# Kernel tuning notes

Hardware: AMD Instinct MI355X
Metric: run time of the kernel (lower is better)

## Reference

```python
import jax, jax.numpy as jnp
import numpy as np

B, N = 32, 512


def _stick_breaking(b, x_mask):
    """Row-major stick-breaking recurrence, O(N^2) sequential steps.

    Equivalent to the TF while_loop: for step in range(N*N), m=step//N, n=step%N:
      fut      = max(0, x_mask[:,m,n+1:] - sum_{m'<m} x[:,m',n+1:])  (col partial sums)
      mfm      = sum_j fut_j
      row_sum  = sum_{n'<n} x[:,m,n']
      col_sum  = sum_{m'<m} x[:,m',n]
      lower    = mask[m,n]*max(0, 1 - row_sum - mfm)
      upper    = mask[m,n]*min(1 - row_sum, 1 - col_sum)
      x[m,n]   = lower + b[m,n]*(upper - lower)
    Key insight: during row m the column partial sums are constant, so the
    future-mass terms for every n can be precomputed as an exclusive reverse
    cumsum; only the within-row dependency (row_sum) needs a scan.
    """
    Bb, Nn, _ = b.shape
    dt = b.dtype

    def row_step(col_sums, inputs):
        b_row, mask_row = inputs                      # [B, N] each
        fut = jnp.maximum(0.0, mask_row - col_sums)   # [B, N]
        # mfm[:, n] = sum_{j > n} fut[:, j]  (exclusive reverse cumsum)
        mfm = jnp.flip(jnp.cumsum(jnp.flip(fut, -1), axis=-1), -1) - fut

        def col_step(row_sum, inp):
            b_mn, m_mn, mfm_n, cs_n = inp             # [B] each
            lower = m_mn * jnp.maximum(0.0, 1.0 - row_sum - mfm_n)
            upper = m_mn * jnp.minimum(1.0 - row_sum, 1.0 - cs_n)
            p = lower + b_mn * (upper - lower)
            return row_sum + p, p

        _, row = jax.lax.scan(
            col_step,
            jnp.zeros((Bb,), dt),
            (b_row.T, mask_row.T, mfm.T, col_sums.T),
        )
        row = row.T                                   # [B, N]
        return col_sums + row, row

    _, rows = jax.lax.scan(
        row_step,
        jnp.zeros((Bb, Nn), dt),
        (jnp.swapaxes(b, 0, 1), jnp.swapaxes(x_mask, 0, 1)),
    )
    return jnp.swapaxes(rows, 0, 1)                   # [B, N, N]


def setup_inputs() -> dict:
    key = jax.random.key(0)
    k1, _ = jax.random.split(key)
    x = jax.random.normal(k1, (B, N, N), dtype=jnp.float32)
    x_mask = jnp.ones((B, N, N), dtype=jnp.float32)
    return {"x": x, "x_mask": x_mask}


def reference(x, x_mask):
    # layer.call applies sigmoid to the logits before stick-breaking
    return _stick_breaking(jax.nn.sigmoid(x), x_mask)
```

## Files before the change

### kernel.cpp

```cpp
#include <hip/hip_runtime.h>

#define NBATCH 32
#define NDIM 512
#define NFAST 448
#define NPAIR 224
#define NWAVE 8


__device__ __forceinline__ float prefix_inc(float x) {
  asm("s_nop 1\n\t"
      "v_add_f32_dpp %0, %0, %0 row_shr:1 row_mask:0xf bank_mask:0xf\n\t"
      "s_nop 1\n\t"
      "v_add_f32_dpp %0, %0, %0 row_shr:2 row_mask:0xf bank_mask:0xf\n\t"
      "s_nop 1\n\t"
      "v_add_f32_dpp %0, %0, %0 row_shr:4 row_mask:0xf bank_mask:0xf\n\t"
      "s_nop 1\n\t"
      "v_add_f32_dpp %0, %0, %0 row_shr:8 row_mask:0xf bank_mask:0xf\n\t"
      "s_nop 1\n\t"
      "v_add_f32_dpp %0, %0, %0 row_bcast:15 row_mask:0xa bank_mask:0xf\n\t"
      "s_nop 1\n\t"
      "v_add_f32_dpp %0, %0, %0 row_bcast:31 row_mask:0xc bank_mask:0xf\n\t"
      "s_nop 1"
      : "+v"(x));
  return x;
}

__device__ __forceinline__ void aff_scan(float& A, float& B) {
  asm("s_nop 1\n\t"
      "v_fmac_f32_dpp %1, %1, %0 row_shr:1 row_mask:0xf bank_mask:0xf\n\t"
      "v_mul_f32_dpp  %0, %0, %0 row_shr:1 row_mask:0xf bank_mask:0xf\n\t"
      "s_nop 0\n\t"
      "v_fmac_f32_dpp %1, %1, %0 row_shr:2 row_mask:0xf bank_mask:0xf\n\t"
      "v_mul_f32_dpp  %0, %0, %0 row_shr:2 row_mask:0xf bank_mask:0xf\n\t"
      "s_nop 0\n\t"
      "v_fmac_f32_dpp %1, %1, %0 row_shr:4 row_mask:0xf bank_mask:0xf\n\t"
      "v_mul_f32_dpp  %0, %0, %0 row_shr:4 row_mask:0xf bank_mask:0xf\n\t"
      "s_nop 0\n\t"
      "v_fmac_f32_dpp %1, %1, %0 row_shr:8 row_mask:0xf bank_mask:0xf\n\t"
      "v_mul_f32_dpp  %0, %0, %0 row_shr:8 row_mask:0xf bank_mask:0xf\n\t"
      "s_nop 0\n\t"
      "v_fmac_f32_dpp %1, %1, %0 row_bcast:15 row_mask:0xa bank_mask:0xf\n\t"
      "v_mul_f32_dpp  %0, %0, %0 row_bcast:15 row_mask:0xa bank_mask:0xf\n\t"
      "s_nop 0\n\t"
      "v_fmac_f32_dpp %1, %1, %0 row_bcast:31 row_mask:0xc bank_mask:0xf\n\t"
      "v_mul_f32_dpp  %0, %0, %0 row_bcast:31 row_mask:0xc bank_mask:0xf\n\t"
      "s_nop 1"
      : "+v"(A), "+v"(B));
}

__device__ __forceinline__ float wave_shr1(float x, float fill) {
  return __int_as_float(__builtin_amdgcn_update_dpp(
      __float_as_int(fill), __float_as_int(x), 0x138 , 0xf, 0xf,
      false));
}

__device__ __forceinline__ void wg_barrier() {
  asm volatile("s_waitcnt lgkmcnt(0)" ::: "memory");
  __builtin_amdgcn_s_barrier();
  asm volatile("" ::: "memory");
}

__global__ __launch_bounds__(512, 2)
void sb_kernel(const float* __restrict__ x, const float* __restrict__ xm,
               float* __restrict__ out) {
  const int tid = (int)threadIdx.x;
  const int lane = tid & 63;
  const int w = __builtin_amdgcn_readfirstlane(tid >> 6);
  const int w3 = 3 * w;
  const size_t base =
      (size_t)blockIdx.x * NDIM * NDIM + (size_t)(w * 64 + lane);
  const float* xb = x + base;
  const float* mb = xm + base;
  float* ob = out + base;

  __shared__ float4 recs[NFAST];
  __shared__ alignas(16) float ex_sa[NWAVE];
  __shared__ alignas(16) float ex_S[NWAVE];
  __shared__ alignas(16) float ex_A[NWAVE];
  __shared__ alignas(16) float ex_B[NWAVE];

  float w8, t8;
  float c2_0, oc2_0, c2_1, oc2_1;
  float c1, c2, oc2;
  float fu = 0.0f, S = 0.0f;

  float X0 = xb[0], M0 = mb[0];
  float X1 = xb[NDIM], M1 = mb[NDIM];
  float Bx0 = xb[2 * NDIM], Bx1 = xb[3 * NDIM];
  float Bm0 = mb[2 * NDIM], Bm1 = mb[3 * NDIM];
  float Cx0 = xb[4 * NDIM], Cx1 = xb[5 * NDIM];
  float Cm0 = mb[4 * NDIM], Cm1 = mb[5 * NDIM];
  float Ax0 = Bx0, Ax1 = Bx1, Am0 = Bm0, Am1 = Bm1;

  {
    float sg0 = __builtin_amdgcn_rcpf(1.0f + __expf(-X0));
    c2_0 = M0 * sg0;
    oc2_0 = 1.0f - c2_0;
    float sg1 = __builtin_amdgcn_rcpf(1.0f + __expf(-X1));
    c2_1 = M1 * sg1;
    oc2_1 = 1.0f - c2_1;
    w8 = 1.0f;
    t8 = c2_0;
  }

  const float* px = xb + (long)(6 - 6 * w) * NDIM;
  const float* pm = mb + (long)(6 - 6 * w) * NDIM;
  float* po = ob - (long)(6 * w) * NDIM;

  auto row_fast = [&](int m, const float4& r, float c2r, float oc2r,
                      float* pO) {
    float PA = prefix_inc(t8);
    float uin = fmaxf(1.0f - (r.z + (PA - t8)), 0.0f);
    bool pW = w8 < uin;
    float A = pW ? 1.0f : oc2r;
    float Bv = pW ? (-t8) : 0.0f;
    aff_scan(A, Bv);
    float Aex = wave_shr1(A, 1.0f);
    float Bex = wave_shr1(Bv, 0.0f);
    if (w < NWAVE - 1 && lane == 63)
      recs[m] = make_float4(A * r.x, fmaf(A, r.y, Bv), r.z + PA, 0.0f);
    float E = r.x + r.y;
    float e = fminf(fmaxf(fmaf(Aex, E, Bex), 0.0f), 1.0f);
    float p = c2r * fminf(e, w8);
    w8 -= p;
    *pO = p;
  };

  auto pair_step = [&](int t, int k, float& WX0, float& WX1, float& WM0,
                       float& WM1, const float& RX0, const float& RX1,
                       const float& RM0, const float& RM1) {
    const int s = t - w3;
    if ((unsigned)s < (unsigned)NPAIR) {
      const int m = 2 * s;
      float4 r0 = make_float4(1.0f, 0.0f, 0.0f, 0.0f), r1 = r0;
      if (w > 0) {
        r0 = recs[m];
        r1 = recs[m + 1];
      }
      const float* pxk = px + (size_t)(2 * k) * NDIM;
      const float* pmk = pm + (size_t)(2 * k) * NDIM;
      WX0 = pxk[0];
      WX1 = pxk[NDIM];
      WM0 = pmk[0];
      WM1 = pmk[NDIM];

      float sg0 = __builtin_amdgcn_rcpf(1.0f + __expf(-RX0));
      float c2n0 = RM0 * sg0;
      float oc2n0 = 1.0f - c2n0;
      float sg1 = __builtin_amdgcn_rcpf(1.0f + __expf(-RX1));
      float c2n1 = RM1 * sg1;
      float oc2n1 = 1.0f - c2n1;

      float* pok = po + (size_t)(2 * k) * NDIM;
      row_fast(m, r0, c2_0, oc2_0, pok);
      t8 = c2_1 * w8;
      row_fast(m + 1, r1, c2_1, oc2_1, pok + NDIM);
      t8 = c2n0 * w8;
      c2_0 = c2n0;
      oc2_0 = oc2n0;
      c2_1 = c2n1;
      oc2_1 = oc2n1;
    }
  };

#pragma unroll 1
  for (int t = 0; t < NPAIR + 3 * (NWAVE - 1); t += 3) {
    pair_step(t + 0, 0, Ax0, Ax1, Am0, Am1, Bx0, Bx1, Bm0, Bm1);
    pair_step(t + 1, 1, Bx0, Bx1, Bm0, Bm1, Cx0, Cx1, Cm0, Cm1);
    pair_step(t + 2, 2, Cx0, Cx1, Cm0, Cm1, Ax0, Ax1, Am0, Am1);
    wg_barrier();
    px += 6 * NDIM;
    pm += 6 * NDIM;
    po += 6 * NDIM;
  }

  float fx0, fm0, fx1, fm1, fx2, fm2, fx3, fm3;
  {
    float m448 = mb[(size_t)448 * NDIM];
    fx1 = xb[(size_t)449 * NDIM];
    fm1 = mb[(size_t)449 * NDIM];
    fx2 = xb[(size_t)450 * NDIM];
    fm2 = mb[(size_t)450 * NDIM];
    fx3 = xb[(size_t)451 * NDIM];
    fm3 = mb[(size_t)451 * NDIM];
    fx0 = fx1;
    fm0 = fm1;
    c2 = c2_0;
    oc2 = oc2_0;
    c1 = m448 - c2;
    float om = 1.0f - m448;
    fu = fmaxf(w8 - om, 0.0f);
    S = fu;
  }

  auto row_full = [&](int m, float& WX, float& WM, const float& RX,
                      const float& RM) {
    const size_t nro = (size_t)((m + 4) & (NDIM - 1)) * NDIM;
    WX = xb[nro];
    WM = mb[nro];

    float PS = prefix_inc(S);
    float PA = prefix_inc(t8);

    if (lane == 63) {
      ex_sa[w] = PA;
      ex_S[w] = PS;
    }
    wg_barrier();

    float4 sl = *(const float4*)&ex_sa[0];
    float4 sh = *(const float4*)&ex_sa[4];
    float4 Sl = *(const float4*)&ex_S[0];
    float4 Sh = *(const float4*)&ex_S[4];
    float off_sa = 0.0f, off_S = 0.0f;
    if (w > 0) { off_sa += sl.x; off_S += Sl.x; }
    if (w > 1) { off_sa += sl.y; off_S += Sl.y; }
    if (w > 2) { off_sa += sl.z; off_S += Sl.z; }
    if (w > 3) { off_sa += sl.w; off_S += Sl.w; }
    if (w > 4) { off_sa += sh.x; off_S += Sh.x; }
    if (w > 5) { off_sa += sh.y; off_S += Sh.y; }
    if (w > 6) { off_sa += sh.z; off_S += Sh.z; }
    float Tg =
        ((Sl.x + Sl.y) + (Sl.z + Sl.w)) + ((Sh.x + Sh.y) + (Sh.z + Sh.w));

    float uin = fmaxf(1.0f - (off_sa + (PA - t8)), 0.0f);
    float R_ = (Tg - off_S) - PS;
    float nc1m = -c1 * R_;

    bool pW = w8 < uin;
    float aP = pW ? 1.0f : oc2;
    float bP = pW ? (-t8) : 0.0f;
    bool pL = (uin - R_) > 0.0f;
    if (pL) {
      aP -= c1;
      bP -= nc1m;
    }

    float A = aP, Bv = bP;
    aff_scan(A, Bv);
    float Aex = wave_shr1(A, 1.0f);
    float Bex = wave_shr1(Bv, 0.0f);

    if (lane == 63) {
      ex_A[w] = A;
      ex_B[w] = Bv;
    }
    wg_barrier();

    float4 Al = *(const float4*)&ex_A[0];
    float4 Ah = *(const float4*)&ex_A[4];
    float4 Bl = *(const float4*)&ex_B[0];
    float4 Bh = *(const float4*)&ex_B[4];
    float E = 1.0f;
    if (w > 0) E = fmaf(Al.x, E, Bl.x);
    if (w > 1) E = fmaf(Al.y, E, Bl.y);
    if (w > 2) E = fmaf(Al.z, E, Bl.z);
    if (w > 3) E = fmaf(Al.w, E, Bl.w);
    if (w > 4) E = fmaf(Ah.x, E, Bh.x);
    if (w > 5) E = fmaf(Ah.y, E, Bh.y);
    if (w > 6) E = fmaf(Ah.z, E, Bh.z);
    float e = fminf(fmaxf(fmaf(Aex, E, Bex), 0.0f), 1.0f);

    float sg = __builtin_amdgcn_rcpf(1.0f + __expf(-RX));
    float c2n = RM * sg;
    float oc2n = 1.0f - c2n;
    float c1n = RM - c2n;
    float omn = 1.0f - RM;

    float U = fminf(e, w8);
    float g = fmaxf(fmaf(c1, e, nc1m), 0.0f);
    float p = fmaf(c2, U, g);
    w8 -= p;
    ob[(size_t)m * NDIM] = p;

    t8 = c2n * w8;
    fu = fmaxf(w8 - omn, 0.0f);
    S = fu;
    c2 = c2n;
    oc2 = oc2n;
    c1 = c1n;
  };

#pragma unroll 1
  for (int m = NFAST; m < NDIM; m += 4) {
    row_full(m + 0, fx0, fm0, fx1, fm1);
    row_full(m + 1, fx1, fm1, fx2, fm2);
    row_full(m + 2, fx2, fm2, fx3, fm3);
    row_full(m + 3, fx3, fm3, fx0, fm0);
  }
}

extern "C" void kernel_launch(void* const* d_in, const int* in_sizes, int n_in,
                              void* d_out, int out_size, void* d_ws,
                              size_t ws_size, hipStream_t stream) {
  const float* x = (const float*)d_in[0];
  const float* xmask = (const float*)d_in[1];
  float* out = (float*)d_out;
  (void)in_sizes;
  (void)n_in;
  (void)out_size;
  (void)d_ws;
  (void)ws_size;
  hipLaunchKernelGGL(sb_kernel, dim3(NBATCH), dim3(512), 0, stream, x, xmask,
                     out);
}
```

Baseline: 250.5 us.

## Process rows in quads per wavefront stage and interleave dual prefix scans

The wavefront-pipelined fast phase now handles four rows per step instead of two, with a two-step skew per wave instead of three, and keeps two register banks of prefetched inputs. This halves the number of stage steps between workgroup barriers relative to rows processed, cutting barrier and pipeline-fill overhead. The full-row phase also merges its two DPP prefix scans into one interleaved asm block so their latencies overlap. The cost is a longer skew in rows per wave and higher register pressure from the extra prefetched rows.

```diff
diff --git a/kernel.cpp b/kernel.cpp
--- a/kernel.cpp
+++ b/kernel.cpp
@@ -3,7 +3,7 @@
 #define NBATCH 32
 #define NDIM 512
 #define NFAST 448
-#define NPAIR 224
+#define NQUAD 112
 #define NWAVE 8
 
 
@@ -23,6 +23,29 @@
       "s_nop 1"
       : "+v"(x));
   return x;
+}
+
+__device__ __forceinline__ void prefix_inc2(float& a, float& b) {
+  asm("s_nop 1\n\t"
+      "v_add_f32_dpp %0, %0, %0 row_shr:1 row_mask:0xf bank_mask:0xf\n\t"
+      "v_add_f32_dpp %1, %1, %1 row_shr:1 row_mask:0xf bank_mask:0xf\n\t"
+      "s_nop 0\n\t"
+      "v_add_f32_dpp %0, %0, %0 row_shr:2 row_mask:0xf bank_mask:0xf\n\t"
+      "v_add_f32_dpp %1, %1, %1 row_shr:2 row_mask:0xf bank_mask:0xf\n\t"
+      "s_nop 0\n\t"
+      "v_add_f32_dpp %0, %0, %0 row_shr:4 row_mask:0xf bank_mask:0xf\n\t"
+      "v_add_f32_dpp %1, %1, %1 row_shr:4 row_mask:0xf bank_mask:0xf\n\t"
+      "s_nop 0\n\t"
+      "v_add_f32_dpp %0, %0, %0 row_shr:8 row_mask:0xf bank_mask:0xf\n\t"
+      "v_add_f32_dpp %1, %1, %1 row_shr:8 row_mask:0xf bank_mask:0xf\n\t"
+      "s_nop 0\n\t"
+      "v_add_f32_dpp %0, %0, %0 row_bcast:15 row_mask:0xa bank_mask:0xf\n\t"
+      "v_add_f32_dpp %1, %1, %1 row_bcast:15 row_mask:0xa bank_mask:0xf\n\t"
+      "s_nop 0\n\t"
+      "v_add_f32_dpp %0, %0, %0 row_bcast:31 row_mask:0xc bank_mask:0xf\n\t"
+      "v_add_f32_dpp %1, %1, %1 row_bcast:31 row_mask:0xc bank_mask:0xf\n\t"
+      "s_nop 1"
+      : "+v"(a), "+v"(b));
 }
 
 __device__ __forceinline__ void aff_scan(float& A, float& B) {
@@ -66,7 +89,7 @@
   const int tid = (int)threadIdx.x;
   const int lane = tid & 63;
   const int w = __builtin_amdgcn_readfirstlane(tid >> 6);
-  const int w3 = 3 * w;
+  const int w2 = 2 * w;
   const size_t base =
       (size_t)blockIdx.x * NDIM * NDIM + (size_t)(w * 64 + lane);
   const float* xb = x + base;
@@ -80,32 +103,39 @@
   __shared__ alignas(16) float ex_B[NWAVE];
 
   float w8, t8;
-  float c2_0, oc2_0, c2_1, oc2_1;
+  float c2_0, oc2_0, c2_1, oc2_1, c2_2, oc2_2, c2_3, oc2_3;
   float c1, c2, oc2;
   float fu = 0.0f, S = 0.0f;
 
-  float X0 = xb[0], M0 = mb[0];
-  float X1 = xb[NDIM], M1 = mb[NDIM];
-  float Bx0 = xb[2 * NDIM], Bx1 = xb[3 * NDIM];
-  float Bm0 = mb[2 * NDIM], Bm1 = mb[3 * NDIM];
-  float Cx0 = xb[4 * NDIM], Cx1 = xb[5 * NDIM];
-  float Cm0 = mb[4 * NDIM], Cm1 = mb[5 * NDIM];
-  float Ax0 = Bx0, Ax1 = Bx1, Am0 = Bm0, Am1 = Bm1;
+  float X0 = xb[0], X1 = xb[NDIM], X2 = xb[2 * NDIM], X3 = xb[3 * NDIM];
+  float M0 = mb[0], M1 = mb[NDIM], M2 = mb[2 * NDIM], M3 = mb[3 * NDIM];
+  float Bx0 = xb[4 * NDIM], Bx1 = xb[5 * NDIM], Bx2 = xb[6 * NDIM],
+        Bx3 = xb[7 * NDIM];
+  float Bm0 = mb[4 * NDIM], Bm1 = mb[5 * NDIM], Bm2 = mb[6 * NDIM],
+        Bm3 = mb[7 * NDIM];
+  float Ax0 = Bx0, Ax1 = Bx1, Ax2 = Bx2, Ax3 = Bx3;
+  float Am0 = Bm0, Am1 = Bm1, Am2 = Bm2, Am3 = Bm3;
 
   {
-    float sg0 = __builtin_amdgcn_rcpf(1.0f + __expf(-X0));
-    c2_0 = M0 * sg0;
+    float s0 = __builtin_amdgcn_rcpf(1.0f + __expf(-X0));
+    float s1 = __builtin_amdgcn_rcpf(1.0f + __expf(-X1));
+    float s2 = __builtin_amdgcn_rcpf(1.0f + __expf(-X2));
+    float s3 = __builtin_amdgcn_rcpf(1.0f + __expf(-X3));
+    c2_0 = M0 * s0;
     oc2_0 = 1.0f - c2_0;
-    float sg1 = __builtin_amdgcn_rcpf(1.0f + __expf(-X1));
-    c2_1 = M1 * sg1;
+    c2_1 = M1 * s1;
     oc2_1 = 1.0f - c2_1;
+    c2_2 = M2 * s2;
+    oc2_2 = 1.0f - c2_2;
+    c2_3 = M3 * s3;
+    oc2_3 = 1.0f - c2_3;
     w8 = 1.0f;
     t8 = c2_0;
   }
 
-  const float* px = xb + (long)(6 - 6 * w) * NDIM;
-  const float* pm = mb + (long)(6 - 6 * w) * NDIM;
-  float* po = ob - (long)(6 * w) * NDIM;
+  const float* px = xb + (long)(8 - 8 * w) * NDIM;
+  const float* pm = mb + (long)(8 - 8 * w) * NDIM;
+  float* po = ob - (long)(8 * w) * NDIM;
 
   auto row_fast = [&](int m, const float4& r, float c2r, float oc2r,
                       float* pO) {
@@ -126,52 +156,72 @@
     *pO = p;
   };
 
-  auto pair_step = [&](int t, int k, float& WX0, float& WX1, float& WM0,
-                       float& WM1, const float& RX0, const float& RX1,
-                       const float& RM0, const float& RM1) {
-    const int s = t - w3;
-    if ((unsigned)s < (unsigned)NPAIR) {
-      const int m = 2 * s;
-      float4 r0 = make_float4(1.0f, 0.0f, 0.0f, 0.0f), r1 = r0;
+  auto quad_step = [&](int t, int k, float& WX0, float& WX1, float& WX2,
+                       float& WX3, float& WM0, float& WM1, float& WM2,
+                       float& WM3, const float& RX0, const float& RX1,
+                       const float& RX2, const float& RX3, const float& RM0,
+                       const float& RM1, const float& RM2, const float& RM3) {
+    const int q = t - w2;
+    if ((unsigned)q < (unsigned)NQUAD) {
+      const int m = 4 * q;
+      float4 r0 = make_float4(1.0f, 0.0f, 0.0f, 0.0f);
+      float4 r1 = r0, r2 = r0, r3 = r0;
       if (w > 0) {
         r0 = recs[m];
         r1 = recs[m + 1];
+        r2 = recs[m + 2];
+        r3 = recs[m + 3];
       }
-      const float* pxk = px + (size_t)(2 * k) * NDIM;
-      const float* pmk = pm + (size_t)(2 * k) * NDIM;
+      const float* pxk = px + (size_t)(4 * k) * NDIM;
+      const float* pmk = pm + (size_t)(4 * k) * NDIM;
       WX0 = pxk[0];
       WX1 = pxk[NDIM];
+      WX2 = pxk[2 * NDIM];
+      WX3 = pxk[3 * NDIM];
       WM0 = pmk[0];
       WM1 = pmk[NDIM];
-
-      float sg0 = __builtin_amdgcn_rcpf(1.0f + __expf(-RX0));
-      float c2n0 = RM0 * sg0;
-      float oc2n0 = 1.0f - c2n0;
-      float sg1 = __builtin_amdgcn_rcpf(1.0f + __expf(-RX1));
-      float c2n1 = RM1 * sg1;
-      float oc2n1 = 1.0f - c2n1;
-
-      float* pok = po + (size_t)(2 * k) * NDIM;
-      row_fast(m, r0, c2_0, oc2_0, pok);
+      WM2 = pmk[2 * NDIM];
+      WM3 = pmk[3 * NDIM];
+
+      float s0 = __builtin_amdgcn_rcpf(1.0f + __expf(-RX0));
+      float s1 = __builtin_amdgcn_rcpf(1.0f + __expf(-RX1));
+      float s2 = __builtin_amdgcn_rcpf(1.0f + __expf(-RX2));
+      float s3 = __builtin_amdgcn_rcpf(1.0f + __expf(-RX3));
+      float c2n0 = RM0 * s0, oc2n0 = 1.0f - c2n0;
+      float c2n1 = RM1 * s1, oc2n1 = 1.0f - c2n1;
+      float c2n2 = RM2 * s2, oc2n2 = 1.0f - c2n2;
+      float c2n3 = RM3 * s3, oc2n3 = 1.0f - c2n3;
+
+      float* pok = po + (size_t)(4 * k) * NDIM;
+      row_fast(m + 0, r0, c2_0, oc2_0, pok);
       t8 = c2_1 * w8;
       row_fast(m + 1, r1, c2_1, oc2_1, pok + NDIM);
+      t8 = c2_2 * w8;
+      row_fast(m + 2, r2, c2_2, oc2_2, pok + 2 * NDIM);
+      t8 = c2_3 * w8;
+      row_fast(m + 3, r3, c2_3, oc2_3, pok + 3 * NDIM);
       t8 = c2n0 * w8;
       c2_0 = c2n0;
       oc2_0 = oc2n0;
       c2_1 = c2n1;
       oc2_1 = oc2n1;
+      c2_2 = c2n2;
+      oc2_2 = oc2n2;
+      c2_3 = c2n3;
+      oc2_3 = oc2n3;
     }
   };
 
 #pragma unroll 1
-  for (int t = 0; t < NPAIR + 3 * (NWAVE - 1); t += 3) {
-    pair_step(t + 0, 0, Ax0, Ax1, Am0, Am1, Bx0, Bx1, Bm0, Bm1);
-    pair_step(t + 1, 1, Bx0, Bx1, Bm0, Bm1, Cx0, Cx1, Cm0, Cm1);
-    pair_step(t + 2, 2, Cx0, Cx1, Cm0, Cm1, Ax0, Ax1, Am0, Am1);
+  for (int t = 0; t < NQUAD + 2 * (NWAVE - 1); t += 2) {
+    quad_step(t + 0, 0, Ax0, Ax1, Ax2, Ax3, Am0, Am1, Am2, Am3, Bx0, Bx1, Bx2,
+              Bx3, Bm0, Bm1, Bm2, Bm3);
+    quad_step(t + 1, 1, Bx0, Bx1, Bx2, Bx3, Bm0, Bm1, Bm2, Bm3, Ax0, Ax1, Ax2,
+              Ax3, Am0, Am1, Am2, Am3);
     wg_barrier();
-    px += 6 * NDIM;
-    pm += 6 * NDIM;
-    po += 6 * NDIM;
+    px += 8 * NDIM;
+    pm += 8 * NDIM;
+    po += 8 * NDIM;
   }
 
   float fx0, fm0, fx1, fm1, fx2, fm2, fx3, fm3;
@@ -199,8 +249,8 @@
     WX = xb[nro];
     WM = mb[nro];
 
-    float PS = prefix_inc(S);
-    float PA = prefix_inc(t8);
+    float PS = S, PA = t8;
+    prefix_inc2(PS, PA);
 
     if (lane == 63) {
       ex_sa[w] = PA;
```

After: 235.6 us. 5.9% less time.
